# Performance work log

Hardware: AMD Instinct MI355X
Metric: run time of the kernel (lower is better)

## Reference

```python
import jax, jax.numpy as jnp
import numpy as np

NUM_HEADS = 4
WINDOW_SIZE = 7
DILATION = 1


def local_mask(height, width, window_size, dilation):
    """[N, N] bool mask: True where token i may attend to token j (dilated 2D window)."""
    radius = window_size // 2
    rows = jnp.arange(height)
    cols = jnp.arange(width)
    r = jnp.repeat(rows, width)          # [N] row index of each flattened token
    c = jnp.tile(cols, height)           # [N] col index of each flattened token
    dr = r[:, None] - r[None, :]         # [N, N]
    dc = c[:, None] - c[None, :]
    within = (jnp.abs(dr) <= radius * dilation) & (jnpp_abs(dc) <= radius * dilation) if False else (
        (jnp.abs(dr) <= radius * dilation) & (jnp.abs(dc) <= radius * dilation)
    )
    on_grid = (dr % dilation == 0) & (dc % dilation == 0)
    return within & on_grid


def setup_inputs() -> dict:
    key = jax.random.key(0)
    kq, kk, kv = jax.random.split(key, 3)
    shape = (2, 64, 64, 64)  # (B, C, H, W)
    q = jax.random.normal(kq, shape, dtype=jnp.float32)
    k = jax.random.normal(kk, shape, dtype=jnp.float32)
    v = jax.random.normal(kv, shape, dtype=jnp.float32)
    return {"q": q, "k": k, "v": v}


def reference(q, k, v):
    B, C, H, W = q.shape
    nh = NUM_HEADS
    hd = C // nh
    N = H * W

    def to_seq(x):
        # (B, C, H, W) -> (B, nh, N, hd)
        x = x.reshape(B, nh, hd, H, W)
        return x.transpose(0, 1, 3, 4, 2).reshape(B, nh, N, hd)

    q_seq = to_seq(q)
    k_seq = to_seq(k)
    v_seq = to_seq(v)

    scale = 1.0 / jnp.sqrt(jnp.asarray(hd, dtype=q.dtype))
    scores = jnp.einsum("bhqd,bhkd->bhqk", q_seq, k_seq) * scale  # [B, nh, N, N]

    mask = local_mask(H, W, WINDOW_SIZE, DILATION)  # [N, N] bool
    neg = jnp.finfo(scores.dtype).min
    scores = jnp.where(mask[None, None, :, :], scores, neg)

    attn = jax.nn.softmax(scores, axis=-1)
    out = jnp.einsum("bhqk,bhkd->bhqd", attn, v_seq)  # [B, nh, N, hd]

    # (B, nh, N, hd) -> (B, C, H, W)
    out = out.reshape(B, nh, H, W, hd).transpose(0, 1, 4, 2, 3).reshape(B, C, H, W)
    return out
```

## Files before the change

### kernel.cpp

```cpp
#include <hip/hip_runtime.h>
#include <hip/hip_bf16.h>
#include <math.h>

#define HD  16
#define HW  4096
#define RAD 3

__global__ __launch_bounds__(512, 2)
void local_attn_kernel(const float* __restrict__ q,
                       const float* __restrict__ k,
                       const float* __restrict__ v,
                       float* __restrict__ out) {
    __shared__ float lds[17408];
    float* ldsK = lds;
    float* ldsV = lds + 8192;

    const int tid = threadIdx.x;
    const int c   = tid & 63;
    const int w   = tid >> 6;

    const int bid = blockIdx.x;
    const int r0  = (bid & 31) * 2;
    const int h   = (bid >> 5) & 3;
    const int b   = bid >> 7;
    const int base = (b * 4 + h) * (HD * HW);

#pragma unroll
    for (int ii = 0; ii < 8; ++ii) {
        int ci = w * 8 + ii;
        int cj = ci & 31;
        const float* src = (ci < 32) ? (k + base) : (v + base);
        float* dst = (ci < 32) ? ldsK : ldsV;
        int s  = cj * 4 + (c >> 4);
        int d  = s >> 3;
        int hr = s & 7;
        int rr = r0 - RAD + hr;
        rr = rr < 0 ? 0 : (rr > 63 ? 63 : rr);
        const float* g = src + d * HW + rr * 64 + (c & 15) * 4;
#if defined(__has_builtin) && __has_builtin(__builtin_amdgcn_global_load_lds)
        __builtin_amdgcn_global_load_lds(
            (const __attribute__((address_space(1))) void*)g,
            (__attribute__((address_space(3))) void*)&dst[cj * 256], 16, 0, 0);
#else
        *(float4*)&dst[cj * 256 + c * 4] = *(const float4*)g;
#endif
    }

    const int pos0 = r0 * 64 + c;
    float qv0[HD], qv1[HD];
#pragma unroll
    for (int d = 0; d < HD; ++d) {
        qv0[d] = q[base + d * HW + pos0] * 0.25f;
        qv1[d] = q[base + d * HW + pos0 + 64] * 0.25f;
    }

    int e2 = (c - RAD) & ~1;
    if (e2 < 0) e2 = 0;
    if (e2 > 56) e2 = 56;
    int lo = c - RAD; if (lo < 0) lo = 0;
    int hi = c + RAD; if (hi > 63) hi = 63;
    const int jlo = lo - e2, jhi = hi - e2;

    __syncthreads();

    const int  rr     = r0 - RAD + w;
    const bool rvalid = ((unsigned)rr < 64u);
    const bool do0    = rvalid && (w <= 6);
    const bool do1    = rvalid && (w >= 1);
    const int  lrow   = w * 64 + e2;

    float s0[8], s1[8];
#pragma unroll
    for (int j = 0; j < 8; ++j) { s0[j] = 0.0f; s1[j] = 0.0f; }

#pragma unroll
    for (int d = 0; d < HD; ++d) {
        const float* kr = &ldsK[d * 512 + lrow];
        float2 k0 = *(const float2*)(kr);
        float2 k1 = *(const float2*)(kr + 2);
        float2 k2 = *(const float2*)(kr + 4);
        float2 k3 = *(const float2*)(kr + 6);
        float q0 = qv0[d], q1 = qv1[d];
        s0[0] = fmaf(q0, k0.x, s0[0]);  s1[0] = fmaf(q1, k0.x, s1[0]);
        s0[1] = fmaf(q0, k0.y, s0[1]);  s1[1] = fmaf(q1, k0.y, s1[1]);
        s0[2] = fmaf(q0, k1.x, s0[2]);  s1[2] = fmaf(q1, k1.x, s1[2]);
        s0[3] = fmaf(q0, k1.y, s0[3]);  s1[3] = fmaf(q1, k1.y, s1[3]);
        s0[4] = fmaf(q0, k2.x, s0[4]);  s1[4] = fmaf(q1, k2.x, s1[4]);
        s0[5] = fmaf(q0, k2.y, s0[5]);  s1[5] = fmaf(q1, k2.y, s1[5]);
        s0[6] = fmaf(q0, k3.x, s0[6]);  s1[6] = fmaf(q1, k3.x, s1[6]);
        s0[7] = fmaf(q0, k3.y, s0[7]);  s1[7] = fmaf(q1, k3.y, s1[7]);
    }

    float l0 = 0.0f, l1 = 0.0f;
#pragma unroll
    for (int j = 0; j < 8; ++j) {
        bool okj = (j >= jlo) && (j <= jhi);
        float e0 = __expf(s0[j]);
        float e1 = __expf(s1[j]);
        e0 = (okj && do0) ? e0 : 0.0f;
        e1 = (okj && do1) ? e1 : 0.0f;
        s0[j] = e0;  s1[j] = e1;
        l0 += e0;    l1 += e1;
    }

    float acc0[HD], acc1[HD];
#pragma unroll
    for (int d = 0; d < HD; ++d) { acc0[d] = 0.0f; acc1[d] = 0.0f; }

#pragma unroll
    for (int d = 0; d < HD; ++d) {
        const float* vr = &ldsV[d * 512 + lrow];
        float2 v0 = *(const float2*)(vr);
        float2 v1 = *(const float2*)(vr + 2);
        float2 v2 = *(const float2*)(vr + 4);
        float2 v3 = *(const float2*)(vr + 6);
        float a0 = acc0[d], a1 = acc1[d];
        a0 = fmaf(s0[0], v0.x, a0);  a1 = fmaf(s1[0], v0.x, a1);
        a0 = fmaf(s0[1], v0.y, a0);  a1 = fmaf(s1[1], v0.y, a1);
        a0 = fmaf(s0[2], v1.x, a0);  a1 = fmaf(s1[2], v1.x, a1);
        a0 = fmaf(s0[3], v1.y, a0);  a1 = fmaf(s1[3], v1.y, a1);
        a0 = fmaf(s0[4], v2.x, a0);  a1 = fmaf(s1[4], v2.x, a1);
        a0 = fmaf(s0[5], v2.y, a0);  a1 = fmaf(s1[5], v2.y, a1);
        a0 = fmaf(s0[6], v3.x, a0);  a1 = fmaf(s1[6], v3.x, a1);
        a0 = fmaf(s0[7], v3.y, a0);  a1 = fmaf(s1[7], v3.y, a1);
        acc0[d] = a0;  acc1[d] = a1;
    }

    __syncthreads();
#pragma unroll
    for (int d = 0; d < HD; ++d) {
        lds[d * 512 + w * 64 + c]         = acc0[d];
        lds[(16 + d) * 512 + w * 64 + c]  = acc1[d];
    }
    lds[16384 + w * 64 + c]       = l0;
    lds[16384 + 512 + w * 64 + c] = l1;
    __syncthreads();

    const int qq = w >> 2;
    const int dq = (w & 3) * 4;
    float lt = 0.0f;
#pragma unroll
    for (int s = 0; s < 8; ++s)
        lt += lds[16384 + qq * 512 + s * 64 + c];
    const float invl = 1.0f / lt;

#pragma unroll
    for (int i = 0; i < 4; ++i) {
        int d = dq + i;
        float a = 0.0f;
#pragma unroll
        for (int s = 0; s < 8; ++s)
            a += lds[(qq * 16 + d) * 512 + s * 64 + c];
        out[base + d * HW + (r0 + qq) * 64 + c] = a * invl;
    }
}

extern "C" void kernel_launch(void* const* d_in, const int* in_sizes, int n_in,
                              void* d_out, int out_size, void* d_ws, size_t ws_size,
                              hipStream_t stream) {
    const float* q = (const float*)d_in[0];
    const float* k = (const float*)d_in[1];
    const float* v = (const float*)d_in[2];
    float* out = (float*)d_out;

    int queries = out_size / HD;
    int blocks  = queries / 128;
    local_attn_kernel<<<blocks, 512, 0, stream>>>(q, k, v, out);
}
```

Before: 10.67 us.

## Replace LDS K/V staging with register loads and DPP lane shifts

```diff
diff --git a/kernel.cpp b/kernel.cpp
--- a/kernel.cpp
+++ b/kernel.cpp
@@ -6,14 +6,31 @@
 #define HW  4096
 #define RAD 3
 
+__device__ __forceinline__ float dpp_shl1(float x) {
+#if defined(__has_builtin) && __has_builtin(__builtin_amdgcn_update_dpp)
+    return __int_as_float(__builtin_amdgcn_update_dpp(
+        0, __float_as_int(x), 0x130 , 0xf, 0xf, true));
+#else
+    int l = (int)(threadIdx.x & 63);
+    return __shfl(x, l + 1, 64);
+#endif
+}
+__device__ __forceinline__ float dpp_shr1(float x) {
+#if defined(__has_builtin) && __has_builtin(__builtin_amdgcn_update_dpp)
+    return __int_as_float(__builtin_amdgcn_update_dpp(
+        0, __float_as_int(x), 0x138 , 0xf, 0xf, true));
+#else
+    int l = (int)(threadIdx.x & 63);
+    return __shfl(x, l - 1, 64);
+#endif
+}
+
 __global__ __launch_bounds__(512, 2)
 void local_attn_kernel(const float* __restrict__ q,
                        const float* __restrict__ k,
                        const float* __restrict__ v,
                        float* __restrict__ out) {
-    __shared__ float lds[17408];
-    float* ldsK = lds;
-    float* ldsV = lds + 8192;
+    __shared__ __align__(16) float mb[512 * 34];
 
     const int tid = threadIdx.x;
     const int c   = tid & 63;
@@ -25,134 +42,97 @@
     const int b   = bid >> 7;
     const int base = (b * 4 + h) * (HD * HW);
 
-#pragma unroll
-    for (int ii = 0; ii < 8; ++ii) {
-        int ci = w * 8 + ii;
-        int cj = ci & 31;
-        const float* src = (ci < 32) ? (k + base) : (v + base);
-        float* dst = (ci < 32) ? ldsK : ldsV;
-        int s  = cj * 4 + (c >> 4);
-        int d  = s >> 3;
-        int hr = s & 7;
-        int rr = r0 - RAD + hr;
-        rr = rr < 0 ? 0 : (rr > 63 ? 63 : rr);
-        const float* g = src + d * HW + rr * 64 + (c & 15) * 4;
-#if defined(__has_builtin) && __has_builtin(__builtin_amdgcn_global_load_lds)
-        __builtin_amdgcn_global_load_lds(
-            (const __attribute__((address_space(1))) void*)g,
-            (__attribute__((address_space(3))) void*)&dst[cj * 256], 16, 0, 0);
-#else
-        *(float4*)&dst[cj * 256 + c * 4] = *(const float4*)g;
-#endif
-    }
+    const int  rr     = r0 - RAD + w;
+    const bool rvalid = ((unsigned)rr < 64u);
+    const bool do0    = rvalid && (w <= 6);
+    const bool do1    = rvalid && (w >= 1);
+    const int  rrc    = rr < 0 ? 0 : (rr > 63 ? 63 : rr);
 
     const int pos0 = r0 * 64 + c;
-    float qv0[HD], qv1[HD];
+    float kd[HD], vd[HD], qv0[HD], qv1[HD];
 #pragma unroll
     for (int d = 0; d < HD; ++d) {
+        kd[d]  = k[base + d * HW + rrc * 64 + c];
+        vd[d]  = v[base + d * HW + rrc * 64 + c];
         qv0[d] = q[base + d * HW + pos0] * 0.25f;
         qv1[d] = q[base + d * HW + pos0 + 64] * 0.25f;
     }
 
-    int e2 = (c - RAD) & ~1;
-    if (e2 < 0) e2 = 0;
-    if (e2 > 56) e2 = 56;
-    int lo = c - RAD; if (lo < 0) lo = 0;
-    int hi = c + RAD; if (hi > 63) hi = 63;
-    const int jlo = lo - e2, jhi = hi - e2;
-
-    __syncthreads();
-
-    const int  rr     = r0 - RAD + w;
-    const bool rvalid = ((unsigned)rr < 64u);
-    const bool do0    = rvalid && (w <= 6);
-    const bool do1    = rvalid && (w >= 1);
-    const int  lrow   = w * 64 + e2;
-
-    float s0[8], s1[8];
+    float s0[7], s1[7];
 #pragma unroll
-    for (int j = 0; j < 8; ++j) { s0[j] = 0.0f; s1[j] = 0.0f; }
+    for (int j = 0; j < 7; ++j) { s0[j] = 0.0f; s1[j] = 0.0f; }
 
 #pragma unroll
     for (int d = 0; d < HD; ++d) {
-        const float* kr = &ldsK[d * 512 + lrow];
-        float2 k0 = *(const float2*)(kr);
-        float2 k1 = *(const float2*)(kr + 2);
-        float2 k2 = *(const float2*)(kr + 4);
-        float2 k3 = *(const float2*)(kr + 6);
-        float q0 = qv0[d], q1 = qv1[d];
-        s0[0] = fmaf(q0, k0.x, s0[0]);  s1[0] = fmaf(q1, k0.x, s1[0]);
-        s0[1] = fmaf(q0, k0.y, s0[1]);  s1[1] = fmaf(q1, k0.y, s1[1]);
-        s0[2] = fmaf(q0, k1.x, s0[2]);  s1[2] = fmaf(q1, k1.x, s1[2]);
-        s0[3] = fmaf(q0, k1.y, s0[3]);  s1[3] = fmaf(q1, k1.y, s1[3]);
-        s0[4] = fmaf(q0, k2.x, s0[4]);  s1[4] = fmaf(q1, k2.x, s1[4]);
-        s0[5] = fmaf(q0, k2.y, s0[5]);  s1[5] = fmaf(q1, k2.y, s1[5]);
-        s0[6] = fmaf(q0, k3.x, s0[6]);  s1[6] = fmaf(q1, k3.x, s1[6]);
-        s0[7] = fmaf(q0, k3.y, s0[7]);  s1[7] = fmaf(q1, k3.y, s1[7]);
+        float kc  = kd[d];
+        float kp1 = dpp_shl1(kc), kp2 = dpp_shl1(kp1), kp3 = dpp_shl1(kp2);
+        float km1 = dpp_shr1(kc), km2 = dpp_shr1(km1), km3 = dpp_shr1(km2);
+        float a0 = qv0[d], a1 = qv1[d];
+        s0[0] = fmaf(a0, km3, s0[0]);  s1[0] = fmaf(a1, km3, s1[0]);
+        s0[1] = fmaf(a0, km2, s0[1]);  s1[1] = fmaf(a1, km2, s1[1]);
+        s0[2] = fmaf(a0, km1, s0[2]);  s1[2] = fmaf(a1, km1, s1[2]);
+        s0[3] = fmaf(a0, kc,  s0[3]);  s1[3] = fmaf(a1, kc,  s1[3]);
+        s0[4] = fmaf(a0, kp1, s0[4]);  s1[4] = fmaf(a1, kp1, s1[4]);
+        s0[5] = fmaf(a0, kp2, s0[5]);  s1[5] = fmaf(a1, kp2, s1[5]);
+        s0[6] = fmaf(a0, kp3, s0[6]);  s1[6] = fmaf(a1, kp3, s1[6]);
     }
 
     float l0 = 0.0f, l1 = 0.0f;
 #pragma unroll
-    for (int j = 0; j < 8; ++j) {
-        bool okj = (j >= jlo) && (j <= jhi);
-        float e0 = __expf(s0[j]);
-        float e1 = __expf(s1[j]);
-        e0 = (okj && do0) ? e0 : 0.0f;
-        e1 = (okj && do1) ? e1 : 0.0f;
-        s0[j] = e0;  s1[j] = e1;
-        l0 += e0;    l1 += e1;
+    for (int j = 0; j < 7; ++j) {
+        bool okc = ((unsigned)(c + j - RAD) < 64u);
+        float p0 = (okc && do0) ? __expf(s0[j]) : 0.0f;
+        float p1 = (okc && do1) ? __expf(s1[j]) : 0.0f;
+        s0[j] = p0;  l0 += p0;
+        s1[j] = p1;  l1 += p1;
     }
 
     float acc0[HD], acc1[HD];
 #pragma unroll
-    for (int d = 0; d < HD; ++d) { acc0[d] = 0.0f; acc1[d] = 0.0f; }
-
-#pragma unroll
     for (int d = 0; d < HD; ++d) {
-        const float* vr = &ldsV[d * 512 + lrow];
-        float2 v0 = *(const float2*)(vr);
-        float2 v1 = *(const float2*)(vr + 2);
-        float2 v2 = *(const float2*)(vr + 4);
-        float2 v3 = *(const float2*)(vr + 6);
-        float a0 = acc0[d], a1 = acc1[d];
-        a0 = fmaf(s0[0], v0.x, a0);  a1 = fmaf(s1[0], v0.x, a1);
-        a0 = fmaf(s0[1], v0.y, a0);  a1 = fmaf(s1[1], v0.y, a1);
-        a0 = fmaf(s0[2], v1.x, a0);  a1 = fmaf(s1[2], v1.x, a1);
-        a0 = fmaf(s0[3], v1.y, a0);  a1 = fmaf(s1[3], v1.y, a1);
-        a0 = fmaf(s0[4], v2.x, a0);  a1 = fmaf(s1[4], v2.x, a1);
-        a0 = fmaf(s0[5], v2.y, a0);  a1 = fmaf(s1[5], v2.y, a1);
-        a0 = fmaf(s0[6], v3.x, a0);  a1 = fmaf(s1[6], v3.x, a1);
-        a0 = fmaf(s0[7], v3.y, a0);  a1 = fmaf(s1[7], v3.y, a1);
+        float vc  = vd[d];
+        float vp1 = dpp_shl1(vc), vp2 = dpp_shl1(vp1), vp3 = dpp_shl1(vp2);
+        float vm1 = dpp_shr1(vc), vm2 = dpp_shr1(vm1), vm3 = dpp_shr1(vm2);
+        float a0, a1;
+        a0 = s0[0] * vm3;            a1 = s1[0] * vm3;
+        a0 = fmaf(s0[1], vm2, a0);   a1 = fmaf(s1[1], vm2, a1);
+        a0 = fmaf(s0[2], vm1, a0);   a1 = fmaf(s1[2], vm1, a1);
+        a0 = fmaf(s0[3], vc,  a0);   a1 = fmaf(s1[3], vc,  a1);
+        a0 = fmaf(s0[4], vp1, a0);   a1 = fmaf(s1[4], vp1, a1);
+        a0 = fmaf(s0[5], vp2, a0);   a1 = fmaf(s1[5], vp2, a1);
+        a0 = fmaf(s0[6], vp3, a0);   a1 = fmaf(s1[6], vp3, a1);
         acc0[d] = a0;  acc1[d] = a1;
     }
 
-    __syncthreads();
+    const int bs = (w * 64 + c) * 34;
 #pragma unroll
-    for (int d = 0; d < HD; ++d) {
-        lds[d * 512 + w * 64 + c]         = acc0[d];
-        lds[(16 + d) * 512 + w * 64 + c]  = acc1[d];
+    for (int d = 0; d < HD; d += 2) {
+        *(float2*)&mb[bs + d]      = make_float2(acc0[d], acc0[d + 1]);
+        *(float2*)&mb[bs + 16 + d] = make_float2(acc1[d], acc1[d + 1]);
     }
-    lds[16384 + w * 64 + c]       = l0;
-    lds[16384 + 512 + w * 64 + c] = l1;
+    *(float2*)&mb[bs + 32] = make_float2(l0, l1);
     __syncthreads();
 
     const int qq = w >> 2;
     const int dq = (w & 3) * 4;
+
     float lt = 0.0f;
 #pragma unroll
     for (int s = 0; s < 8; ++s)
-        lt += lds[16384 + qq * 512 + s * 64 + c];
+        lt += mb[(s * 64 + c) * 34 + 32 + qq];
     const float invl = 1.0f / lt;
 
+    float a[4] = {0.0f, 0.0f, 0.0f, 0.0f};
 #pragma unroll
-    for (int i = 0; i < 4; ++i) {
-        int d = dq + i;
-        float a = 0.0f;
+    for (int s = 0; s < 8; ++s) {
+        const int rb = (s * 64 + c) * 34 + qq * 16 + dq;
+        float2 x0 = *(const float2*)&mb[rb];
+        float2 x1 = *(const float2*)&mb[rb + 2];
+        a[0] += x0.x;  a[1] += x0.y;  a[2] += x1.x;  a[3] += x1.y;
+    }
 #pragma unroll
-        for (int s = 0; s < 8; ++s)
-            a += lds[(qq * 16 + d) * 512 + s * 64 + c];
-        out[base + d * HW + (r0 + qq) * 64 + c] = a * invl;
-    }
+    for (int i = 0; i < 4; ++i)
+        out[base + (dq + i) * HW + (r0 + qq) * 64 + c] = a[i] * invl;
 }
 
 extern "C" void kernel_launch(void* const* d_in, const int* in_sizes, int n_in,
```

Result: faster. 10.23 us, median of 2 (-4.1%).
